# Kernel optimization log

Hardware: AMD Instinct MI355X
Metric: run time of the kernel (lower is better)

Reference implementation:

```python
import jax, jax.numpy as jnp
import numpy as np

B, N, C = 8, 2048, 1024
SPARSITY = 0.8
K_KEEP = int(N * SPARSITY)  # 1638
NEG = 1e10


def setup_inputs() -> dict:
    key = jax.random.key(0)
    ks = jax.random.split(key, 7)
    s = 1.0 / np.sqrt(C)
    return {
        "x": jax.random.normal(ks[0], (B, N, C), dtype=jnp.float32),
        "Wq": jax.random.uniform(ks[1], (C, C), dtype=jnp.float32, minval=-s, maxval=s),
        "bq": jax.random.uniform(ks[2], (C,), dtype=jnp.float32, minval=-s, maxval=s),
        "Wk": jax.random.uniform(ks[3], (C, C), dtype=jnp.float32, minval=-s, maxval=s),
        "bk": jax.random.uniform(ks[4], (C,), dtype=jnp.float32, minval=-s, maxval=s),
        "Wv": jax.random.uniform(ks[5], (C, C), dtype=jnp.float32, minval=-s, maxval=s),
        "bv": jax.random.uniform(ks[6], (C,), dtype=jnp.float32, minval=-s, maxval=s),
    }


def reference(x, Wq, bq, Wk, bk, Wv, bv):
    # Linear projections (torch Linear: y = x @ W.T + b)
    Q = jnp.einsum("bnc,dc->bnd", x, Wq) + bq
    Kt = jnp.einsum("bnc,dc->bnd", x, Wk) + bk
    V = jnp.einsum("bnc,dc->bnd", x, Wv) + bv
    attn = jnp.einsum("bnd,bmd->bnm", Q, Kt) / jnp.sqrt(jnp.float32(C))  # [B,N,N]
    _, idx = jax.lax.top_k(attn, K_KEEP)  # idx: [B,N,K_KEEP]
    bI = jnp.arange(B)[:, None, None]
    nI = jnp.arange(N)[None, :, None]
    mask = jnp.zeros_like(attn).at[bI, nI, idx].set(1.0)
    attn = attn * mask - NEG * (1.0 - mask)
    attn = jax.nn.softmax(attn, axis=-1)
    return jnp.einsum("bnm,bmd->bnd", attn, V)
```

## Files before the change

kernel.cpp:

```cpp
#include <hip/hip_runtime.h>

typedef _Float16 f16;
typedef __attribute__((ext_vector_type(8))) _Float16 f16x8;
typedef __attribute__((ext_vector_type(4))) _Float16 f16x4;
typedef __attribute__((ext_vector_type(4))) float f32x4;

constexpr int BB = 8;
constexpr int NN = 2048;
constexpr int CC = 1024;
constexpr int MTOT = BB * NN;
constexpr int KKEEP = 1638;

__device__ __forceinline__ void gl_lds16(const void* g, void* l) {
  __builtin_amdgcn_global_load_lds((__attribute__((address_space(1))) void*)g,
                                   (__attribute__((address_space(3))) void*)l,
                                   16, 0, 0);
}

constexpr int X4 = MTOT * CC / 4;
constexpr int W4 = CC * CC / 4;
__global__ __launch_bounds__(256) void cvt_all(
    const float* __restrict__ x, const float* __restrict__ Wq,
    const float* __restrict__ Wk, const float* __restrict__ Wv,
    f16* __restrict__ xb, f16* __restrict__ wqkv) {
  int i = blockIdx.x * 256 + threadIdx.x;
  const float* s;
  f16* d;
  if (i < X4) { s = x; d = xb; }
  else if (i < X4 + W4) { i -= X4; s = Wq; d = wqkv; }
  else if (i < X4 + 2 * W4) { i -= X4 + W4; s = Wk; d = wqkv + CC * CC; }
  else { i -= X4 + 2 * W4; s = Wv; d = wqkv + 2 * CC * CC; }
  float4 f = ((const float4*)s)[i];
  f16x4 o = {(f16)f.x, (f16)f.y, (f16)f.z, (f16)f.w};
  ((f16x4*)d)[i] = o;
}

template <int MODE>
__global__ __launch_bounds__(256, 2) void gemm_bt(
    const f16* __restrict__ A, const f16* __restrict__ B,
    const float* __restrict__ b0, const float* __restrict__ b1,
    const float* __restrict__ b2, void* __restrict__ Cout,
    void* __restrict__ Cout2, int K, int lda, int ldb, int ldc, float scale,
    long strideA, long strideB, long strideC) {
  const f16* Ab = A + (size_t)blockIdx.z * strideA;
  const f16* Bbp = B + (size_t)blockIdx.z * strideB;

  const int bm = blockIdx.x * 128;
  const int bn = blockIdx.y * 128;
  const int tid = threadIdx.x;
  const int wave = tid >> 6;
  const int lane = tid & 63;
  const int wy = wave >> 1, wx = wave & 1;

  __shared__ f16 As[128 * 64];
  __shared__ f16 Bs[128 * 64];

  f32x4 acc[4][4];
#pragma unroll
  for (int i = 0; i < 4; i++)
#pragma unroll
    for (int j = 0; j < 4; j++) acc[i][j] = (f32x4){0.f, 0.f, 0.f, 0.f};

  const int sr = wave * 32 + (lane >> 3);
  const int gsrc = ((lane & 7) ^ ((lane >> 3) & 7)) * 8;
  const f16* gA0 = Ab + (size_t)(bm + sr) * lda + gsrc;
  const f16* gB0 = Bbp + (size_t)(bn + sr) * ldb + gsrc;
  f16* lA = As + (wave * 32) * 64 + lane * 8;
  f16* lB = Bs + (wave * 32) * 64 + lane * 8;

  const int id = lane & 15;
  const int q = lane >> 4;
  const int frm0 = wy * 64 + id;
  const int frn0 = wx * 64 + id;
  const int g0 = (q ^ (id & 7)) * 8;
  const int g1 = ((q + 4) ^ (id & 7)) * 8;

  for (int k0 = 0; k0 < K; k0 += 64) {
#pragma unroll
    for (int r = 0; r < 4; r++) {
      gl_lds16(gA0 + (size_t)8 * r * lda + k0, lA + r * 512);
      gl_lds16(gB0 + (size_t)8 * r * ldb + k0, lB + r * 512);
    }
    __syncthreads();
    f16x8 av[2][4], bv[2][4];
#pragma unroll
    for (int i = 0; i < 4; i++) {
      av[0][i] = *(const f16x8*)(As + (frm0 + 16 * i) * 64 + g0);
      av[1][i] = *(const f16x8*)(As + (frm0 + 16 * i) * 64 + g1);
      bv[0][i] = *(const f16x8*)(Bs + (frn0 + 16 * i) * 64 + g0);
      bv[1][i] = *(const f16x8*)(Bs + (frn0 + 16 * i) * 64 + g1);
    }
#pragma unroll
    for (int kk = 0; kk < 2; kk++)
#pragma unroll
      for (int i = 0; i < 4; i++)
#pragma unroll
        for (int j = 0; j < 4; j++)
          acc[i][j] = __builtin_amdgcn_mfma_f32_16x16x32_f16(av[kk][i], bv[kk][j],
                                                             acc[i][j], 0, 0, 0);
    __syncthreads();
  }

  const int ci = id;
#pragma unroll
  for (int i = 0; i < 4; i++) {
#pragma unroll
    for (int j = 0; j < 4; j++) {
      const int row0 = bm + wy * 64 + i * 16 + q * 4;
      const int col = bn + wx * 64 + j * 16 + ci;
      if (MODE == 0) {
        float* C = (float*)Cout + (size_t)blockIdx.z * strideC;
#pragma unroll
        for (int r = 0; r < 4; r++)
          C[(size_t)(row0 + r) * ldc + col] = acc[i][j][r] * scale;
      } else {
        if (bn < 2048) {
          f16* C = (f16*)Cout;
          const float* bias = (bn < 1024) ? b0 : (b1 - 1024);
          const float bb = bias[col];
#pragma unroll
          for (int r = 0; r < 4; r++)
            C[(size_t)(row0 + r) * 2048 + col] = (f16)(acc[i][j][r] + bb);
        } else {
          f16* C = (f16*)Cout2;
          const float bb = b2[col - 2048];
          f16x4 o;
#pragma unroll
          for (int r = 0; r < 4; r++) o[r] = (f16)(acc[i][j][r] + bb);
          *(f16x4*)(C + (size_t)(col - 2048) * MTOT + row0) = o;
        }
      }
    }
  }
}

__global__ __launch_bounds__(256) void topk_softmax_kernel(
    const float* __restrict__ S, f16* __restrict__ P) {
  const size_t row = blockIdx.x;
  const float* srow = S + row * 2048;
  f16* prow = P + row * 2048;
  const int t = threadIdx.x;
  const int lane = t & 63;
  const int wave = t >> 6;

  float v[8];
  float4 f0 = ((const float4*)srow)[2 * t];
  float4 f1 = ((const float4*)srow)[2 * t + 1];
  v[0] = f0.x; v[1] = f0.y; v[2] = f0.z; v[3] = f0.w;
  v[4] = f1.x; v[5] = f1.y; v[6] = f1.z; v[7] = f1.w;

  __shared__ float wlo[4], whi[4];
  __shared__ float wf[4];
  __shared__ int wagg[4];
  __shared__ int hist[2048];
  __shared__ float cval[128];
  __shared__ int cidx[128];
  __shared__ int cnum;
  __shared__ int sh_thr, sh_want;

  float lo = v[0], hi = v[0];
#pragma unroll
  for (int j = 1; j < 8; j++) { lo = fminf(lo, v[j]); hi = fmaxf(hi, v[j]); }
#pragma unroll
  for (int off = 32; off > 0; off >>= 1) {
    lo = fminf(lo, __shfl_xor(lo, off, 64));
    hi = fmaxf(hi, __shfl_xor(hi, off, 64));
  }
  if (lane == 0) { wlo[wave] = lo; whi[wave] = hi; }
  if (t == 0) cnum = 0;
  ((int4*)hist)[2 * t] = (int4){0, 0, 0, 0};
  ((int4*)hist)[2 * t + 1] = (int4){0, 0, 0, 0};
  __syncthreads();
  lo = fminf(fminf(wlo[0], wlo[1]), fminf(wlo[2], wlo[3]));
  hi = fmaxf(fmaxf(whi[0], whi[1]), fmaxf(whi[2], whi[3]));

  if (hi == lo) {
    const float w = 1.0f / (float)KKEEP;
    f16x8 o;
#pragma unroll
    for (int j = 0; j < 8; j++) o[j] = (f16)((t * 8 + j < KKEEP) ? w : 0.f);
    *(f16x8*)(prow + t * 8) = o;
    return;
  }

  const float qs = 2048.0f / (hi - lo);
  int key[8];
#pragma unroll
  for (int j = 0; j < 8; j++) {
    int k = (int)((v[j] - lo) * qs);
    key[j] = (k > 2047) ? 2047 : k;
  }
#pragma unroll
  for (int j = 0; j < 8; j++) atomicAdd(&hist[key[j]], 1);
  __syncthreads();

  int4 h0 = ((const int4*)hist)[2 * t];
  int4 h1 = ((const int4*)hist)[2 * t + 1];
  int h[8] = {h0.x, h0.y, h0.z, h0.w, h1.x, h1.y, h1.z, h1.w};
  int s[8];
  s[7] = h[7];
#pragma unroll
  for (int j = 6; j >= 0; j--) s[j] = s[j + 1] + h[j];
  const int partial = s[0];
  int sfx = partial;
#pragma unroll
  for (int off = 1; off < 64; off <<= 1) {
    int o = __shfl_down(sfx, off, 64);
    sfx += (lane + off < 64) ? o : 0;
  }
  if (lane == 0) wagg[wave] = sfx;
  __syncthreads();
  int hiw = 0;
#pragma unroll
  for (int w = 0; w < 4; w++) hiw += (w > wave) ? wagg[w] : 0;
  const int base = (sfx - partial) + hiw;
#pragma unroll
  for (int j = 0; j < 8; j++) {
    const int cum = s[j] + base;
    const int above = cum - h[j];
    if (cum >= KKEEP && above < KKEEP) {
      sh_thr = 8 * t + j;
      sh_want = KKEEP - above;
    }
  }
  __syncthreads();
  const int thr = sh_thr;
  const int wantin = sh_want;

#pragma unroll
  for (int j = 0; j < 8; j++) {
    if (key[j] == thr) {
      int slot = atomicAdd(&cnum, 1);
      if (slot < 128) { cval[slot] = v[j]; cidx[slot] = t * 8 + j; }
    }
  }
  __syncthreads();
  const int n = (cnum < 128) ? cnum : 128;

  float e[8];
  float lsum = 0.f;
#pragma unroll
  for (int j = 0; j < 8; j++) {
    bool kept;
    if (key[j] > thr) {
      kept = true;
    } else if (key[j] < thr) {
      kept = false;
    } else {
      const int myidx = t * 8 + j;
      int rank = 0;
      for (int c = 0; c < n; c++) {
        const float cv = cval[c];
        rank += (cv > v[j] || (cv == v[j] && cidx[c] < myidx)) ? 1 : 0;
      }
      kept = rank < wantin;
    }
    e[j] = kept ? __expf(v[j] - hi) : 0.f;
    lsum += e[j];
  }
#pragma unroll
  for (int off = 32; off > 0; off >>= 1) lsum += __shfl_xor(lsum, off, 64);
  if (lane == 0) wf[wave] = lsum;
  __syncthreads();
  const float inv = 1.0f / (wf[0] + wf[1] + wf[2] + wf[3]);

  f16x8 o;
#pragma unroll
  for (int j = 0; j < 8; j++) o[j] = (f16)(e[j] * inv);
  *(f16x8*)(prow + t * 8) = o;
}

extern "C" void kernel_launch(void* const* d_in, const int* in_sizes, int n_in,
                              void* d_out, int out_size, void* d_ws, size_t ws_size,
                              hipStream_t stream) {
  (void)in_sizes; (void)n_in; (void)out_size; (void)ws_size;
  const float* x = (const float*)d_in[0];
  const float* Wq = (const float*)d_in[1];
  const float* bq = (const float*)d_in[2];
  const float* Wk = (const float*)d_in[3];
  const float* bk = (const float*)d_in[4];
  const float* Wv = (const float*)d_in[5];
  const float* bv = (const float*)d_in[6];
  float* out = (float*)d_out;

  char* ws = (char*)d_ws;
  f16* qkb = (f16*)(ws + 0);
  f16* vtb = (f16*)(ws + 67108864);
  float* S = (float*)(ws + 100663296);
  f16* xb = (f16*)(ws + 100663296);
  f16* wqkv = (f16*)(ws + 134217728);
  f16* Pc = (f16*)(ws + 0);

  cvt_all<<<(X4 + 3 * W4 + 255) / 256, 256, 0, stream>>>(x, Wq, Wk, Wv, xb, wqkv);

  gemm_bt<3><<<dim3(MTOT / 128, 3072 / 128, 1), 256, 0, stream>>>(
      xb, wqkv, bq, bk, bv, qkb, vtb, CC, CC, CC, 0, 1.f, 0, 0, 0);

  gemm_bt<0><<<dim3(NN / 128, NN / 128, BB), 256, 0, stream>>>(
      qkb, qkb + 1024, nullptr, nullptr, nullptr, S, nullptr, CC, 2048, 2048, NN,
      1.f / 32.f, (long)NN * 2048, (long)NN * 2048, (long)NN * NN);

  topk_softmax_kernel<<<MTOT, 256, 0, stream>>>(S, Pc);

  gemm_bt<0><<<dim3(NN / 128, CC / 128, BB), 256, 0, stream>>>(
      Pc, vtb, nullptr, nullptr, nullptr, out, nullptr, NN, NN, MTOT, CC, 1.f,
      (long)NN * NN, (long)NN, (long)NN * CC);
}
```

Measured before the change: 439.1 us.

## Restructure GEMM into 256x256 tiles with double-buffered LDS and ping-pong scheduling

Replaces the 128x128, 4-wave GEMM with a 256x256, 8-wave kernel. It double-buffers LDS and loads the next tiles in half-tile stages, interleaved with MFMA quadrants under explicit barriers, waitcnts, sched_barriers and setprio. The goal is to hide global-to-LDS latency behind matrix math and raise data reuse per block. The cost is 64KB of LDS per block and a larger accumulator. Fewer blocks are launched, which may leave tail or occupancy problems on the smaller GEMMs.

Measured after the change: 435.0 us. Within noise of the previous version (-0.9%).

```diff
diff --git a/kernel.cpp b/kernel.cpp
--- a/kernel.cpp
+++ b/kernel.cpp
@@ -35,8 +35,38 @@
   ((f16x4*)d)[i] = o;
 }
 
+#define SBAR __builtin_amdgcn_sched_barrier(0)
+
+#define STAGE_A(buf, h, tt)                                              \
+  {                                                                      \
+    gl_lds16(gA + (size_t)((h) * 128) * lda + (tt) * 64,                 \
+             lA + (buf) * 16384 + (h) * 8192);                           \
+    gl_lds16(gA + (size_t)((h) * 128 + 8) * lda + (tt) * 64,             \
+             lA + (buf) * 16384 + (h) * 8192 + 512);                     \
+  }
+#define STAGE_B(buf, h, tt)                                              \
+  {                                                                      \
+    gl_lds16(gB + (size_t)((h) * 128) * ldb + (tt) * 64,                 \
+             lB + (buf) * 16384 + (h) * 8192);                           \
+    gl_lds16(gB + (size_t)((h) * 128 + 8) * ldb + (tt) * 64,             \
+             lB + (buf) * 16384 + (h) * 8192 + 512);                     \
+  }
+
+#define MFMA_Q(qm, qn)                                                   \
+  {                                                                      \
+    __builtin_amdgcn_s_setprio(1);                                       \
+    _Pragma("unroll") for (int kk = 0; kk < 2; kk++)                     \
+    _Pragma("unroll") for (int ii = 0; ii < 4; ii++)                     \
+    _Pragma("unroll") for (int jj = 0; jj < 2; jj++)                     \
+        acc[(qm) * 4 + ii][(qn) * 2 + jj] =                              \
+            __builtin_amdgcn_mfma_f32_16x16x32_f16(                      \
+                av[kk][ii], bv[kk][(qn) * 2 + jj],                       \
+                acc[(qm) * 4 + ii][(qn) * 2 + jj], 0, 0, 0);             \
+    __builtin_amdgcn_s_setprio(0);                                       \
+  }
+
 template <int MODE>
-__global__ __launch_bounds__(256, 2) void gemm_bt(
+__global__ __launch_bounds__(512, 2) void gemm_bt(
     const f16* __restrict__ A, const f16* __restrict__ B,
     const float* __restrict__ b0, const float* __restrict__ b1,
     const float* __restrict__ b2, void* __restrict__ Cout,
@@ -45,69 +75,128 @@
   const f16* Ab = A + (size_t)blockIdx.z * strideA;
   const f16* Bbp = B + (size_t)blockIdx.z * strideB;
 
-  const int bm = blockIdx.x * 128;
-  const int bn = blockIdx.y * 128;
+  const int bm = blockIdx.x * 256;
+  const int bn = blockIdx.y * 256;
   const int tid = threadIdx.x;
   const int wave = tid >> 6;
   const int lane = tid & 63;
-  const int wy = wave >> 1, wx = wave & 1;
-
-  __shared__ f16 As[128 * 64];
-  __shared__ f16 Bs[128 * 64];
-
-  f32x4 acc[4][4];
-#pragma unroll
-  for (int i = 0; i < 4; i++)
+  const int wy = wave >> 2;
+  const int wx = wave & 3;
+
+  __shared__ __attribute__((aligned(16))) f16 As[2 * 256 * 64];
+  __shared__ __attribute__((aligned(16))) f16 Bs[2 * 256 * 64];
+
+  f32x4 acc[8][4];
+#pragma unroll
+  for (int i = 0; i < 8; i++)
 #pragma unroll
     for (int j = 0; j < 4; j++) acc[i][j] = (f32x4){0.f, 0.f, 0.f, 0.f};
 
-  const int sr = wave * 32 + (lane >> 3);
+  const int srow = wave * 16 + (lane >> 3);
   const int gsrc = ((lane & 7) ^ ((lane >> 3) & 7)) * 8;
-  const f16* gA0 = Ab + (size_t)(bm + sr) * lda + gsrc;
-  const f16* gB0 = Bbp + (size_t)(bn + sr) * ldb + gsrc;
-  f16* lA = As + (wave * 32) * 64 + lane * 8;
-  f16* lB = Bs + (wave * 32) * 64 + lane * 8;
+  const f16* gA = Ab + (size_t)(bm + srow) * lda + gsrc;
+  const f16* gB = Bbp + (size_t)(bn + srow) * ldb + gsrc;
+  f16* lA = As + wave * 1024 + lane * 8;
+  f16* lB = Bs + wave * 1024 + lane * 8;
+
+  const int NT = K >> 6;
+
+  STAGE_A(0, 0, 0);
+  STAGE_B(0, 0, 0);
+  STAGE_A(0, 1, 0);
+  STAGE_B(0, 1, 0);
+  if (NT > 1) {
+    STAGE_A(1, 0, 1);
+    STAGE_B(1, 0, 1);
+    asm volatile("s_waitcnt vmcnt(8)");
+  } else {
+    asm volatile("s_waitcnt vmcnt(4)");
+  }
+  SBAR;
+  __builtin_amdgcn_s_barrier();
+  SBAR;
 
   const int id = lane & 15;
   const int q = lane >> 4;
-  const int frm0 = wy * 64 + id;
-  const int frn0 = wx * 64 + id;
-  const int g0 = (q ^ (id & 7)) * 8;
-  const int g1 = ((q + 4) ^ (id & 7)) * 8;
-
-  for (int k0 = 0; k0 < K; k0 += 64) {
-#pragma unroll
-    for (int r = 0; r < 4; r++) {
-      gl_lds16(gA0 + (size_t)8 * r * lda + k0, lA + r * 512);
-      gl_lds16(gB0 + (size_t)8 * r * ldb + k0, lB + r * 512);
-    }
-    __syncthreads();
-    f16x8 av[2][4], bv[2][4];
-#pragma unroll
-    for (int i = 0; i < 4; i++) {
-      av[0][i] = *(const f16x8*)(As + (frm0 + 16 * i) * 64 + g0);
-      av[1][i] = *(const f16x8*)(As + (frm0 + 16 * i) * 64 + g1);
-      bv[0][i] = *(const f16x8*)(Bs + (frn0 + 16 * i) * 64 + g0);
-      bv[1][i] = *(const f16x8*)(Bs + (frn0 + 16 * i) * 64 + g1);
-    }
-#pragma unroll
-    for (int kk = 0; kk < 2; kk++)
-#pragma unroll
-      for (int i = 0; i < 4; i++)
-#pragma unroll
-        for (int j = 0; j < 4; j++)
-          acc[i][j] = __builtin_amdgcn_mfma_f32_16x16x32_f16(av[kk][i], bv[kk][j],
-                                                             acc[i][j], 0, 0, 0);
-    __syncthreads();
-  }
-
-  const int ci = id;
-#pragma unroll
-  for (int i = 0; i < 4; i++) {
+  const int g0 = (q ^ (lane & 7)) * 8;
+  const int g1 = ((q + 4) ^ (lane & 7)) * 8;
+  const int aoff = (wy * 64 + id) * 64;
+  const int boff = (wx * 32 + id) * 64;
+
+  for (int t = 0; t < NT; ++t) {
+    const int cur = t & 1;
+    const f16* Ac = As + cur * 16384;
+    const f16* Bc = Bs + cur * 16384;
+    f16x8 av[2][4];
+    f16x8 bv[2][4];
+
+#pragma unroll
+    for (int ii = 0; ii < 4; ii++) {
+      av[0][ii] = *(const f16x8*)(Ac + ii * 1024 + aoff + g0);
+      av[1][ii] = *(const f16x8*)(Ac + ii * 1024 + aoff + g1);
+    }
+#pragma unroll
+    for (int jj = 0; jj < 2; jj++) {
+      bv[0][jj] = *(const f16x8*)(Bc + jj * 1024 + boff + g0);
+      bv[1][jj] = *(const f16x8*)(Bc + jj * 1024 + boff + g1);
+    }
+    if (t + 1 < NT) STAGE_A(cur ^ 1, 1, t + 1);
+    SBAR;
+    __builtin_amdgcn_s_barrier();
+    SBAR;
+    MFMA_Q(0, 0);
+    SBAR;
+    if (t + 1 < NT) asm volatile("s_waitcnt vmcnt(6)");
+    else            asm volatile("s_waitcnt vmcnt(0)");
+    __builtin_amdgcn_s_barrier();
+    SBAR;
+
+#pragma unroll
+    for (int jj = 0; jj < 2; jj++) {
+      bv[0][2 + jj] = *(const f16x8*)(Bc + (128 + jj * 16) * 64 + boff + g0);
+      bv[1][2 + jj] = *(const f16x8*)(Bc + (128 + jj * 16) * 64 + boff + g1);
+    }
+    if (t + 1 < NT) STAGE_B(cur ^ 1, 1, t + 1);
+    SBAR;
+    __builtin_amdgcn_s_barrier();
+    SBAR;
+    MFMA_Q(0, 1);
+    SBAR;
+    __builtin_amdgcn_s_barrier();
+    SBAR;
+
+#pragma unroll
+    for (int ii = 0; ii < 4; ii++) {
+      av[0][ii] = *(const f16x8*)(Ac + (128 + ii * 16) * 64 + aoff + g0);
+      av[1][ii] = *(const f16x8*)(Ac + (128 + ii * 16) * 64 + aoff + g1);
+    }
+    if (t + 2 < NT) STAGE_A(cur, 0, t + 2);
+    SBAR;
+    __builtin_amdgcn_s_barrier();
+    SBAR;
+    MFMA_Q(1, 0);
+    SBAR;
+    __builtin_amdgcn_s_barrier();
+    SBAR;
+
+    if (t + 2 < NT) STAGE_B(cur, 0, t + 2);
+    SBAR;
+    __builtin_amdgcn_s_barrier();
+    SBAR;
+    MFMA_Q(1, 1);
+    SBAR;
+    if (t + 2 < NT)      asm volatile("s_waitcnt vmcnt(8)");
+    else if (t + 1 < NT) asm volatile("s_waitcnt vmcnt(4)");
+    __builtin_amdgcn_s_barrier();
+    SBAR;
+  }
+
+#pragma unroll
+  for (int i = 0; i < 8; i++) {
+    const int row0 = bm + (i >> 2) * 128 + wy * 64 + (i & 3) * 16 + q * 4;
 #pragma unroll
     for (int j = 0; j < 4; j++) {
-      const int row0 = bm + wy * 64 + i * 16 + q * 4;
-      const int col = bn + wx * 64 + j * 16 + ci;
+      const int col = bn + (j >> 1) * 128 + wx * 32 + (j & 1) * 16 + id;
       if (MODE == 0) {
         float* C = (float*)Cout + (size_t)blockIdx.z * strideC;
 #pragma unroll
@@ -293,16 +382,16 @@
 
   cvt_all<<<(X4 + 3 * W4 + 255) / 256, 256, 0, stream>>>(x, Wq, Wk, Wv, xb, wqkv);
 
-  gemm_bt<3><<<dim3(MTOT / 128, 3072 / 128, 1), 256, 0, stream>>>(
+  gemm_bt<3><<<dim3(MTOT / 256, 3072 / 256, 1), 512, 0, stream>>>(
       xb, wqkv, bq, bk, bv, qkb, vtb, CC, CC, CC, 0, 1.f, 0, 0, 0);
 
-  gemm_bt<0><<<dim3(NN / 128, NN / 128, BB), 256, 0, stream>>>(
+  gemm_bt<0><<<dim3(NN / 256, NN / 256, BB), 512, 0, stream>>>(
       qkb, qkb + 1024, nullptr, nullptr, nullptr, S, nullptr, CC, 2048, 2048, NN,
       1.f / 32.f, (long)NN * 2048, (long)NN * 2048, (long)NN * NN);
 
   topk_softmax_kernel<<<MTOT, 256, 0, stream>>>(S, Pc);
 
-  gemm_bt<0><<<dim3(NN / 128, CC / 128, BB), 256, 0, stream>>>(
+  gemm_bt<0><<<dim3(NN / 256, CC / 256, BB), 512, 0, stream>>>(
       Pc, vtb, nullptr, nullptr, nullptr, out, nullptr, NN, NN, MTOT, CC, 1.f,
       (long)NN * NN, (long)NN, (long)NN * CC);
 }
```

## Process one top-k softmax row per wavefront instead of per block

Applied to the files above, without the earlier changes.

Restructures the top-k/softmax kernel so each 64-lane wave handles a full row, holding 32 values per lane. This removes all block-level barriers and LDS cross-wave reductions, using wave shuffles and lgkmcnt waits instead. The histogram shrinks to 1024 bins per wave and the candidate buffer to 64 entries. Keys are recomputed rather than stored, to limit register use. The cost is higher register pressure and a larger risk of candidate-buffer overflow in dense bins.

Result: slower. 454.9 us (+3.6%).

```diff
diff --git a/kernel.cpp b/kernel.cpp
--- a/kernel.cpp
+++ b/kernel.cpp
@@ -136,71 +136,73 @@
 
 __global__ __launch_bounds__(256) void topk_softmax_kernel(
     const float* __restrict__ S, f16* __restrict__ P) {
-  const size_t row = blockIdx.x;
+  const int tid = threadIdx.x;
+  const int wave = tid >> 6;
+  const int lane = tid & 63;
+  const size_t row = (size_t)blockIdx.x * 4 + wave;
   const float* srow = S + row * 2048;
   f16* prow = P + row * 2048;
-  const int t = threadIdx.x;
-  const int lane = t & 63;
-  const int wave = t >> 6;
-
-  float v[8];
-  float4 f0 = ((const float4*)srow)[2 * t];
-  float4 f1 = ((const float4*)srow)[2 * t + 1];
-  v[0] = f0.x; v[1] = f0.y; v[2] = f0.z; v[3] = f0.w;
-  v[4] = f1.x; v[5] = f1.y; v[6] = f1.z; v[7] = f1.w;
-
-  __shared__ float wlo[4], whi[4];
-  __shared__ float wf[4];
-  __shared__ int wagg[4];
-  __shared__ int hist[2048];
-  __shared__ float cval[128];
-  __shared__ int cidx[128];
-  __shared__ int cnum;
-  __shared__ int sh_thr, sh_want;
+
+  __shared__ int hist_s[4][1024];
+  __shared__ float cval_s[4][64];
+  __shared__ int cidx_s[4][64];
+  __shared__ int cnum_s[4];
+  __shared__ int thr_s[4], want_s[4];
+  int* hist = hist_s[wave];
+
+  float v[32];
+#pragma unroll
+  for (int r = 0; r < 8; r++) {
+    float4 f = ((const float4*)srow)[lane + 64 * r];
+    v[4 * r] = f.x; v[4 * r + 1] = f.y; v[4 * r + 2] = f.z; v[4 * r + 3] = f.w;
+  }
+
+#pragma unroll
+  for (int r = 0; r < 4; r++) ((int4*)hist)[lane + 64 * r] = (int4){0, 0, 0, 0};
+  if (lane == 0) cnum_s[wave] = 0;
 
   float lo = v[0], hi = v[0];
 #pragma unroll
-  for (int j = 1; j < 8; j++) { lo = fminf(lo, v[j]); hi = fmaxf(hi, v[j]); }
+  for (int j = 1; j < 32; j++) { lo = fminf(lo, v[j]); hi = fmaxf(hi, v[j]); }
 #pragma unroll
   for (int off = 32; off > 0; off >>= 1) {
     lo = fminf(lo, __shfl_xor(lo, off, 64));
     hi = fmaxf(hi, __shfl_xor(hi, off, 64));
   }
-  if (lane == 0) { wlo[wave] = lo; whi[wave] = hi; }
-  if (t == 0) cnum = 0;
-  ((int4*)hist)[2 * t] = (int4){0, 0, 0, 0};
-  ((int4*)hist)[2 * t + 1] = (int4){0, 0, 0, 0};
-  __syncthreads();
-  lo = fminf(fminf(wlo[0], wlo[1]), fminf(wlo[2], wlo[3]));
-  hi = fmaxf(fmaxf(whi[0], whi[1]), fmaxf(whi[2], whi[3]));
 
   if (hi == lo) {
     const float w = 1.0f / (float)KKEEP;
-    f16x8 o;
-#pragma unroll
-    for (int j = 0; j < 8; j++) o[j] = (f16)((t * 8 + j < KKEEP) ? w : 0.f);
-    *(f16x8*)(prow + t * 8) = o;
+#pragma unroll
+    for (int r = 0; r < 8; r++) {
+      const int e0 = 4 * lane + 256 * r;
+      f16x4 o;
+#pragma unroll
+      for (int c = 0; c < 4; c++) o[c] = (f16)((e0 + c < KKEEP) ? w : 0.f);
+      *(f16x4*)(prow + e0) = o;
+    }
     return;
   }
 
-  const float qs = 2048.0f / (hi - lo);
-  int key[8];
-#pragma unroll
-  for (int j = 0; j < 8; j++) {
+  const float qs = 1024.0f / (hi - lo);
+  asm volatile("s_waitcnt lgkmcnt(0)" ::: "memory");
+#pragma unroll
+  for (int j = 0; j < 32; j++) {
     int k = (int)((v[j] - lo) * qs);
-    key[j] = (k > 2047) ? 2047 : k;
-  }
-#pragma unroll
-  for (int j = 0; j < 8; j++) atomicAdd(&hist[key[j]], 1);
-  __syncthreads();
-
-  int4 h0 = ((const int4*)hist)[2 * t];
-  int4 h1 = ((const int4*)hist)[2 * t + 1];
-  int h[8] = {h0.x, h0.y, h0.z, h0.w, h1.x, h1.y, h1.z, h1.w};
-  int s[8];
-  s[7] = h[7];
-#pragma unroll
-  for (int j = 6; j >= 0; j--) s[j] = s[j + 1] + h[j];
+    k = (k > 1023) ? 1023 : k;
+    atomicAdd(&hist[k], 1);
+  }
+  asm volatile("s_waitcnt lgkmcnt(0)" ::: "memory");
+
+  int h[16];
+#pragma unroll
+  for (int r = 0; r < 4; r++) {
+    int4 t4 = ((const int4*)hist)[4 * lane + r];
+    h[4 * r] = t4.x; h[4 * r + 1] = t4.y; h[4 * r + 2] = t4.z; h[4 * r + 3] = t4.w;
+  }
+  int s[16];
+  s[15] = h[15];
+#pragma unroll
+  for (int j = 14; j >= 0; j--) s[j] = s[j + 1] + h[j];
   const int partial = s[0];
   int sfx = partial;
 #pragma unroll
@@ -208,66 +210,69 @@
     int o = __shfl_down(sfx, off, 64);
     sfx += (lane + off < 64) ? o : 0;
   }
-  if (lane == 0) wagg[wave] = sfx;
-  __syncthreads();
-  int hiw = 0;
-#pragma unroll
-  for (int w = 0; w < 4; w++) hiw += (w > wave) ? wagg[w] : 0;
-  const int base = (sfx - partial) + hiw;
-#pragma unroll
-  for (int j = 0; j < 8; j++) {
+  const int base = sfx - partial;
+#pragma unroll
+  for (int j = 0; j < 16; j++) {
     const int cum = s[j] + base;
     const int above = cum - h[j];
     if (cum >= KKEEP && above < KKEEP) {
-      sh_thr = 8 * t + j;
-      sh_want = KKEEP - above;
-    }
-  }
-  __syncthreads();
-  const int thr = sh_thr;
-  const int wantin = sh_want;
-
-#pragma unroll
-  for (int j = 0; j < 8; j++) {
-    if (key[j] == thr) {
-      int slot = atomicAdd(&cnum, 1);
-      if (slot < 128) { cval[slot] = v[j]; cidx[slot] = t * 8 + j; }
-    }
-  }
-  __syncthreads();
-  const int n = (cnum < 128) ? cnum : 128;
-
-  float e[8];
+      thr_s[wave] = 16 * lane + j;
+      want_s[wave] = KKEEP - above;
+    }
+  }
+  asm volatile("s_waitcnt lgkmcnt(0)" ::: "memory");
+  const int thr = thr_s[wave];
+  const int wantin = want_s[wave];
+
+#pragma unroll
+  for (int j = 0; j < 32; j++) {
+    int k = (int)((v[j] - lo) * qs);
+    k = (k > 1023) ? 1023 : k;
+    if (k == thr) {
+      int slot = atomicAdd(&cnum_s[wave], 1);
+      if (slot < 64) {
+        cval_s[wave][slot] = v[j];
+        cidx_s[wave][slot] = 4 * lane + 256 * (j >> 2) + (j & 3);
+      }
+    }
+  }
+  asm volatile("s_waitcnt lgkmcnt(0)" ::: "memory");
+  const int n = (cnum_s[wave] < 64) ? cnum_s[wave] : 64;
+
   float lsum = 0.f;
 #pragma unroll
-  for (int j = 0; j < 8; j++) {
+  for (int j = 0; j < 32; j++) {
+    int k = (int)((v[j] - lo) * qs);
+    k = (k > 1023) ? 1023 : k;
     bool kept;
-    if (key[j] > thr) {
+    if (k > thr) {
       kept = true;
-    } else if (key[j] < thr) {
+    } else if (k < thr) {
       kept = false;
     } else {
-      const int myidx = t * 8 + j;
+      const int myidx = 4 * lane + 256 * (j >> 2) + (j & 3);
       int rank = 0;
       for (int c = 0; c < n; c++) {
-        const float cv = cval[c];
-        rank += (cv > v[j] || (cv == v[j] && cidx[c] < myidx)) ? 1 : 0;
+        const float cv = cval_s[wave][c];
+        rank += (cv > v[j] || (cv == v[j] && cidx_s[wave][c] < myidx)) ? 1 : 0;
       }
       kept = rank < wantin;
     }
-    e[j] = kept ? __expf(v[j] - hi) : 0.f;
-    lsum += e[j];
+    const float e = kept ? __expf(v[j] - hi) : 0.f;
+    v[j] = e;
+    lsum += e;
   }
 #pragma unroll
   for (int off = 32; off > 0; off >>= 1) lsum += __shfl_xor(lsum, off, 64);
-  if (lane == 0) wf[wave] = lsum;
-  __syncthreads();
-  const float inv = 1.0f / (wf[0] + wf[1] + wf[2] + wf[3]);
-
-  f16x8 o;
-#pragma unroll
-  for (int j = 0; j < 8; j++) o[j] = (f16)(e[j] * inv);
-  *(f16x8*)(prow + t * 8) = o;
+  const float inv = 1.0f / lsum;
+
+#pragma unroll
+  for (int r = 0; r < 8; r++) {
+    f16x4 o;
+#pragma unroll
+    for (int c = 0; c < 4; c++) o[c] = (f16)(v[4 * r + c] * inv);
+    *(f16x4*)(prow + 4 * lane + 256 * r) = o;
+  }
 }
 
 extern "C" void kernel_launch(void* const* d_in, const int* in_sizes, int n_in,
@@ -300,7 +305,7 @@
       qkb, qkb + 1024, nullptr, nullptr, nullptr, S, nullptr, CC, 2048, 2048, NN,
       1.f / 32.f, (long)NN * 2048, (long)NN * 2048, (long)NN * NN);
 
-  topk_softmax_kernel<<<MTOT, 256, 0, stream>>>(S, Pc);
+  topk_softmax_kernel<<<MTOT / 4, 256, 0, stream>>>(S, Pc);
 
   gemm_bt<0><<<dim3(NN / 128, CC / 128, BB), 256, 0, stream>>>(
       Pc, vtb, nullptr, nullptr, nullptr, out, nullptr, NN, NN, MTOT, CC, 1.f,
```
